# Performance work log

Measured on AMD Instinct MI355X. Metric: run time of the kernel, lower is better.

The kernel has to match this reference:

```python
import jax, jax.numpy as jnp
import numpy as np

TOKEN_VOCAB = 512   # token id range used for packing ngram tuples into ints
VOCAB_SIZE = 50000  # max ngram vocab per size (ngram_to_size values)
NGRAM_SIZES = (2, 3)
OOV_ID = 0
ID_OFFSET = 4       # vocab ids start at 4 (idx + 4 in _get_top_ngrams)


def _make_table(rng, n):
    # Build a sorted, unique packed-key table emulating the dict produced by
    # _get_top_ngrams: {ngram_tuple: idx+4}. Keys packed base-TOKEN_VOCAB.
    cand = rng.integers(0, TOKEN_VOCAB, size=(VOCAB_SIZE * 3, n), dtype=np.int64)
    packed = np.zeros(cand.shape[0], dtype=np.int64)
    for j in range(n):
        packed = packed * TOKEN_VOCAB + cand[:, j]
    uniq = np.unique(packed)[:VOCAB_SIZE]
    keys = np.sort(uniq)
    vals = np.arange(keys.shape[0], dtype=np.int64) + ID_OFFSET
    return jnp.asarray(keys), jnp.asarray(vals)


def setup_inputs() -> dict:
    key = jax.random.key(0)
    x = jax.random.randint(key, (256, 8192), 0, TOKEN_VOCAB, dtype=jnp.int64)
    rng = np.random.default_rng(0)
    keys2, vals2 = _make_table(rng, 2)
    keys3, vals3 = _make_table(rng, 3)
    return {"x": x, "keys2": keys2, "vals2": vals2, "keys3": keys3, "vals3": vals3}


def _encode_ngram_ids(x, keys, vals, n):
    # Left-pad with 0 by (n-1), sliding windows of length n per position,
    # pack each window into a single int key, then sorted-table lookup
    # (semantically equal to lookup_table.get(tuple(window), 0)).
    B, S = x.shape
    padded = jnp.pad(x, ((0, 0), (n - 1, 0)))  # [B, S+n-1]
    packed = jnp.zeros((B, S), dtype=jnp.int64)
    for j in range(n):  # tiny fixed loop over window offset
        packed = packed * TOKEN_VOCAB + padded[:, j:j + S]
    pos = jnp.clip(jnp.searchsorted(keys, packed.ravel()), 0, keys.shape[0] - 1)
    hit = keys[pos] == packed.ravel()
    ids = jnp.where(hit, vals[pos], OOV_ID)
    return ids.reshape(B, S)


def reference(x, keys2, vals2, keys3, vals3):
    tables = {2: (keys2, vals2), 3: (keys3, vals3)}
    per_n = [_encode_ngram_ids(x, *tables[n], n) for n in NGRAM_SIZES]
    return jnp.stack(per_n, axis=0)  # [n_sizes, B, S]
```

## Files before the change

kernel.cpp:

```cpp
#include <hip/hip_runtime.h>


#define TOKEN_VOCAB 512
#define SHIFT3 10
#define NBUCKET3 (1 << 17)
#define DIRECT2_ENTRIES (TOKEN_VOCAB * TOKEN_VOCAB)

__global__ void build_direct2(const int* __restrict__ keys2,
                              const int* __restrict__ vals2, int K2,
                              int* __restrict__ direct2) {
    int i = blockIdx.x * blockDim.x + threadIdx.x;
    if (i < K2) direct2[keys2[i]] = vals2[i];
}

__global__ void build_start3(const int* __restrict__ keys3, int K3,
                             int* __restrict__ start3) {
    int b = blockIdx.x * blockDim.x + threadIdx.x;
    if (b > NBUCKET3) return;
    int target = b << SHIFT3;
    int lo = 0, hi = K3;
    while (lo < hi) {
        int mid = (lo + hi) >> 1;
        if (keys3[mid] < target) lo = mid + 1; else hi = mid;
    }
    start3[b] = lo;
}

__global__ void ngram_encode_fast(const int* __restrict__ x,
                                  const int* __restrict__ direct2,
                                  const int* __restrict__ start3,
                                  const int* __restrict__ keys3,
                                  const int* __restrict__ vals3,
                                  int* __restrict__ out, int total, int S) {
    int base = (blockIdx.x * blockDim.x + threadIdx.x) * 4;
    if (base >= total) return;
    int s = base & (S - 1);
    const int4 cur = *(const int4*)(x + base);
    int tm1 = (s >= 1) ? x[base - 1] : 0;
    int tm2 = (s >= 1) ? x[base - 2] : 0;
    int t[6] = {tm2, tm1, cur.x, cur.y, cur.z, cur.w};

    int o2[4], o3[4];
    int k3v[4], blo[4], bhi[4];
    #pragma unroll
    for (int j = 0; j < 4; ++j) {
        int k2 = t[j + 1] * TOKEN_VOCAB + t[j + 2];
        int k3 = (t[j] * TOKEN_VOCAB + t[j + 1]) * TOKEN_VOCAB + t[j + 2];
        k3v[j] = k3;
        o2[j] = direct2[k2];
        int b = k3 >> SHIFT3;
        blo[j] = start3[b];
        bhi[j] = start3[b + 1];
    }
    #pragma unroll
    for (int j = 0; j < 4; ++j) {
        int v = 0;
        for (int p = blo[j]; p < bhi[j]; ++p) {
            int kv = keys3[p];
            if (kv >= k3v[j]) { v = (kv == k3v[j]) ? vals3[p] : 0; break; }
        }
        o3[j] = v;
    }
    *(int4*)(out + base)         = make_int4(o2[0], o2[1], o2[2], o2[3]);
    *(int4*)(out + total + base) = make_int4(o3[0], o3[1], o3[2], o3[3]);
}

__device__ __forceinline__ int table_lookup(const int* __restrict__ keys,
                                            const int* __restrict__ vals,
                                            int K, int packed) {
    int lo = 0, hi = K;
    while (lo < hi) {
        int mid = (lo + hi) >> 1;
        if (keys[mid] < packed) lo = mid + 1; else hi = mid;
    }
    int pos = lo < (K - 1) ? lo : (K - 1);
    return (keys[pos] == packed) ? vals[pos] : 0;
}

__global__ void ngram_encode_kernel(const int* __restrict__ x,
                                    const int* __restrict__ keys2,
                                    const int* __restrict__ vals2, int K2,
                                    const int* __restrict__ keys3,
                                    const int* __restrict__ vals3, int K3,
                                    int* __restrict__ out, int total, int S) {
    int idx = blockIdx.x * blockDim.x + threadIdx.x;
    if (idx >= total) return;
    int s = idx & (S - 1);
    int t0 = x[idx];
    int t1 = (s >= 1) ? x[idx - 1] : 0;
    int t2 = (s >= 2) ? x[idx - 2] : 0;
    int k2 = t1 * TOKEN_VOCAB + t0;
    int k3 = (t2 * TOKEN_VOCAB + t1) * TOKEN_VOCAB + t0;
    out[idx]         = table_lookup(keys2, vals2, K2, k2);
    out[total + idx] = table_lookup(keys3, vals3, K3, k3);
}

extern "C" void kernel_launch(void* const* d_in, const int* in_sizes, int n_in,
                              void* d_out, int out_size, void* d_ws, size_t ws_size,
                              hipStream_t stream) {
    const int* x     = (const int*)d_in[0];
    const int* keys2 = (const int*)d_in[1];
    const int* vals2 = (const int*)d_in[2];
    const int* keys3 = (const int*)d_in[3];
    const int* vals3 = (const int*)d_in[4];
    int* out = (int*)d_out;

    const int total = in_sizes[0];
    const int S = 8192;
    const int K2 = in_sizes[1];
    const int K3 = in_sizes[3];

    const size_t ws_needed = (size_t)(DIRECT2_ENTRIES + NBUCKET3 + 1) * sizeof(int);
    if (ws_size >= ws_needed) {
        int* direct2 = (int*)d_ws;
        int* start3  = direct2 + DIRECT2_ENTRIES;

        hipMemsetAsync(direct2, 0, DIRECT2_ENTRIES * sizeof(int), stream);
        build_direct2<<<(K2 + 255) / 256, 256, 0, stream>>>(keys2, vals2, K2, direct2);
        build_start3<<<(NBUCKET3 + 1 + 255) / 256, 256, 0, stream>>>(keys3, K3, start3);

        const int block = 256;
        const int elems = total / 4;
        ngram_encode_fast<<<(elems + block - 1) / block, block, 0, stream>>>(
            x, direct2, start3, keys3, vals3, out, total, S);
    } else {
        const int block = 256;
        ngram_encode_kernel<<<(total + block - 1) / block, block, 0, stream>>>(
            x, keys2, vals2, K2, keys3, vals3, K3, out, total, S);
    }
}
```

Before: 100.9 us.

## Replace bucketed sorted search for trigrams with open-addressing hash table

```diff
diff --git a/kernel.cpp b/kernel.cpp
--- a/kernel.cpp
+++ b/kernel.cpp
@@ -2,35 +2,39 @@
 
 
 #define TOKEN_VOCAB 512
-#define SHIFT3 10
-#define NBUCKET3 (1 << 17)
 #define DIRECT2_ENTRIES (TOKEN_VOCAB * TOKEN_VOCAB)
+#define LOG_NSLOT3 18
+#define NSLOT3 (1 << LOG_NSLOT3)
+#define MASK3 (NSLOT3 - 1)
 
-__global__ void build_direct2(const int* __restrict__ keys2,
-                              const int* __restrict__ vals2, int K2,
-                              int* __restrict__ direct2) {
+__device__ __forceinline__ unsigned hash3(int k) {
+    return ((unsigned)k * 2654435761u) >> (32 - LOG_NSLOT3);
+}
+
+__global__ void build_tables(const int* __restrict__ keys2,
+                             const int* __restrict__ vals2, int K2,
+                             const int* __restrict__ keys3,
+                             const int* __restrict__ vals3, int K3,
+                             int* __restrict__ direct2,
+                             int* __restrict__ kt3,
+                             int* __restrict__ vt3) {
     int i = blockIdx.x * blockDim.x + threadIdx.x;
     if (i < K2) direct2[keys2[i]] = vals2[i];
-}
-
-__global__ void build_start3(const int* __restrict__ keys3, int K3,
-                             int* __restrict__ start3) {
-    int b = blockIdx.x * blockDim.x + threadIdx.x;
-    if (b > NBUCKET3) return;
-    int target = b << SHIFT3;
-    int lo = 0, hi = K3;
-    while (lo < hi) {
-        int mid = (lo + hi) >> 1;
-        if (keys3[mid] < target) lo = mid + 1; else hi = mid;
+    if (i < K3) {
+        int k = keys3[i];
+        unsigned h = hash3(k);
+        for (;;) {
+            int prev = atomicCAS(&kt3[h], -1, k);
+            if (prev == -1) { vt3[h] = vals3[i]; break; }
+            h = (h + 1) & MASK3;
+        }
     }
-    start3[b] = lo;
 }
 
 __global__ void ngram_encode_fast(const int* __restrict__ x,
                                   const int* __restrict__ direct2,
-                                  const int* __restrict__ start3,
-                                  const int* __restrict__ keys3,
-                                  const int* __restrict__ vals3,
+                                  const int* __restrict__ kt3,
+                                  const int* __restrict__ vt3,
                                   int* __restrict__ out, int total, int S) {
     int base = (blockIdx.x * blockDim.x + threadIdx.x) * 4;
     if (base >= total) return;
@@ -40,24 +44,28 @@
     int tm2 = (s >= 1) ? x[base - 2] : 0;
     int t[6] = {tm2, tm1, cur.x, cur.y, cur.z, cur.w};
 
-    int o2[4], o3[4];
-    int k3v[4], blo[4], bhi[4];
+    int k3v[4], d2[4], kx[4];
+    unsigned h[4];
     #pragma unroll
     for (int j = 0; j < 4; ++j) {
         int k2 = t[j + 1] * TOKEN_VOCAB + t[j + 2];
         int k3 = (t[j] * TOKEN_VOCAB + t[j + 1]) * TOKEN_VOCAB + t[j + 2];
         k3v[j] = k3;
-        o2[j] = direct2[k2];
-        int b = k3 >> SHIFT3;
-        blo[j] = start3[b];
-        bhi[j] = start3[b + 1];
+        h[j]   = hash3(k3);
+        d2[j]  = direct2[k2];
+        kx[j]  = kt3[h[j]];
     }
+    int o2[4], o3[4];
     #pragma unroll
     for (int j = 0; j < 4; ++j) {
+        o2[j] = (d2[j] < 0) ? 0 : d2[j];
         int v = 0;
-        for (int p = blo[j]; p < bhi[j]; ++p) {
-            int kv = keys3[p];
-            if (kv >= k3v[j]) { v = (kv == k3v[j]) ? vals3[p] : 0; break; }
+        int k = kx[j];
+        unsigned hh = h[j];
+        while (k != -1) {
+            if (k == k3v[j]) { v = vt3[hh]; break; }
+            hh = (hh + 1) & MASK3;
+            k = kt3[hh];
         }
         o3[j] = v;
     }
@@ -110,19 +118,23 @@
     const int K2 = in_sizes[1];
     const int K3 = in_sizes[3];
 
-    const size_t ws_needed = (size_t)(DIRECT2_ENTRIES + NBUCKET3 + 1) * sizeof(int);
+    const size_t ws_needed = (size_t)(DIRECT2_ENTRIES + 2 * NSLOT3) * sizeof(int);
     if (ws_size >= ws_needed) {
         int* direct2 = (int*)d_ws;
-        int* start3  = direct2 + DIRECT2_ENTRIES;
+        int* kt3     = direct2 + DIRECT2_ENTRIES;
+        int* vt3     = kt3 + NSLOT3;
 
-        hipMemsetAsync(direct2, 0, DIRECT2_ENTRIES * sizeof(int), stream);
-        build_direct2<<<(K2 + 255) / 256, 256, 0, stream>>>(keys2, vals2, K2, direct2);
-        build_start3<<<(NBUCKET3 + 1 + 255) / 256, 256, 0, stream>>>(keys3, K3, start3);
+        hipMemsetAsync(d_ws, 0xFF,
+                       (size_t)(DIRECT2_ENTRIES + NSLOT3) * sizeof(int), stream);
+
+        const int kmax = (K2 > K3) ? K2 : K3;
+        build_tables<<<(kmax + 255) / 256, 256, 0, stream>>>(
+            keys2, vals2, K2, keys3, vals3, K3, direct2, kt3, vt3);
 
         const int block = 256;
         const int elems = total / 4;
         ngram_encode_fast<<<(elems + block - 1) / block, block, 0, stream>>>(
-            x, direct2, start3, keys3, vals3, out, total, S);
+            x, direct2, kt3, vt3, out, total, S);
     } else {
         const int block = 256;
         ngram_encode_kernel<<<(total + block - 1) / block, block, 0, stream>>>(
```

After: 102.8 us. Within noise of the previous version (+1.8%).
